# Kernel tuning notes

Hardware: AMD Instinct MI355X
Metric: run time of the kernel (lower is better)

Reference implementation:

```python
import jax, jax.numpy as jnp
import numpy as np

HEADS = 8
DIM_HEAD = 64
DIM = 512
HIDDEN = HEADS * DIM_HEAD  # 512


def setup_inputs() -> dict:
    key = jax.random.key(0)
    k1, k2, k3, k4 = jax.random.split(key, 4)
    B, H, W = 8, 64, 64
    x = jax.random.normal(k1, (B, DIM, H, W), dtype=jnp.float32)
    # Conv2d 1x1 weights stored as [out_ch, in_ch] (kernel 1x1 squeezed)
    w_qkv = jax.random.normal(k2, (3 * HIDDEN, DIM), dtype=jnp.float32) * (1.0 / np.sqrt(DIM))
    w_out = jax.random.normal(k3, (DIM, HIDDEN), dtype=jnp.float32) * (1.0 / np.sqrt(HIDDEN))
    b_out = jax.random.normal(k4, (DIM,), dtype=jnp.float32) * 0.01
    return {"x": x, "w_qkv": w_qkv, "w_out": w_out, "b_out": b_out}


def reference(x, w_qkv, w_out, b_out):
    b, c, h, w = x.shape
    n = h * w
    # to_qkv: 1x1 conv == channel GEMM
    qkv = jnp.einsum('bchw,oc->bohw', x, w_qkv)               # [b, 3*heads*dh, h, w]
    qkv = qkv.reshape(b, 3, HEADS, DIM_HEAD, n)               # split (qkv heads c), flatten (h w)
    q, k, v = qkv[:, 0], qkv[:, 1], qkv[:, 2]                 # each [b, heads, dh, n]
    k = jax.nn.softmax(k, axis=-1)                            # softmax over spatial tokens
    context = jnp.einsum('bhdn,bhen->bhde', k, v)             # [b, heads, dh, dh]
    out = jnp.einsum('bhde,bhdn->bhen', context, q)           # [b, heads, dh, n]
    out = out.reshape(b, HIDDEN, h, w)
    # to_out: 1x1 conv with bias
    return jnp.einsum('bchw,oc->bohw', out, w_out) + b_out[None, :, None, None]
```

## Files before the change

### kernel.cpp

```cpp
#include <hip/hip_runtime.h>
#include <hip/hip_bf16.h>


typedef __attribute__((ext_vector_type(8))) __bf16 bf16x8;
typedef __attribute__((ext_vector_type(4))) float f32x4;
typedef __attribute__((ext_vector_type(8))) unsigned short u16x8;
typedef __attribute__((ext_vector_type(4))) float float4v;

__device__ __forceinline__ unsigned short f2b(float f) {
  unsigned int u = __builtin_bit_cast(unsigned int, f);
  unsigned int r = (u + 0x7FFFu + ((u >> 16) & 1u)) >> 16;
  return (unsigned short)r;
}
__device__ __forceinline__ float b2f(unsigned short h) {
  unsigned int u = ((unsigned int)h) << 16;
  return __builtin_bit_cast(float, u);
}

__global__ __launch_bounds__(256) void prep_wkv_kernel(const float* __restrict__ w,
                                                       unsigned short* __restrict__ wkv) {
  int i = (blockIdx.x * 256 + threadIdx.x) * 4;
  const float* src = w + 512 * 512;
  #pragma unroll
  for (int j = 0; j < 4; ++j) wkv[i + j] = f2b(src[i + j]);
}

__global__ __launch_bounds__(256) void prep_wqT_kernel(const float* __restrict__ w,
                                                       unsigned short* __restrict__ WqT) {
  __shared__ unsigned short tile[64][65];
  const int ct = blockIdx.x, ot = blockIdx.y;
  const int c0 = ct * 64, o0 = ot * 64;
  const int tc = threadIdx.x & 63, tr = threadIdx.x >> 6;
  #pragma unroll
  for (int i = 0; i < 16; ++i) {
    int row = tr * 16 + i;
    tile[tc][row] = f2b(w[(long)(o0 + row) * 512 + c0 + tc]);
  }
  __syncthreads();
  #pragma unroll
  for (int i = 0; i < 16; ++i) {
    int row = tr * 16 + i;
    WqT[(long)(c0 + row) * 512 + o0 + tc] = tile[row][tc];
  }
}

__global__ __launch_bounds__(256) void transpose_x_kernel(const float* __restrict__ x,
                                                          unsigned short* __restrict__ xT) {
  __shared__ unsigned short tile[64][65];
  const int b = blockIdx.z, ct = blockIdx.y, nt = blockIdx.x;
  const int c0 = ct * 64, n0 = nt * 64;
  const int tid = threadIdx.x;

  const int n_off = (tid & 15) * 4;
  const float* xp = x + ((long)b * 512) * 4096 + n0;
  #pragma unroll
  for (int i = 0; i < 4; ++i) {
    int c_local = i * 16 + (tid >> 4);
    float4v v = *(const float4v*)(xp + (long)(c0 + c_local) * 4096 + n_off);
    #pragma unroll
    for (int j = 0; j < 4; ++j) tile[n_off + j][c_local] = f2b(v[j]);
  }
  __syncthreads();

  const int n_row = tid >> 2;
  const int c_seg = (tid & 3) * 16;
  unsigned short* xtp = xT + ((long)b * 4096 + n0 + n_row) * 512 + c0 + c_seg;
  #pragma unroll
  for (int s = 0; s < 2; ++s) {
    u16x8 o;
    #pragma unroll
    for (int k = 0; k < 8; ++k) o[k] = tile[n_row][c_seg + s * 8 + k];
    *(u16x8*)(xtp + s * 8) = o;
  }
}

__global__ __launch_bounds__(256) void gemm128_bt(
    const unsigned short* __restrict__ A, long strideA,
    const unsigned short* __restrict__ BT, long strideBT,
    void* __restrict__ Cout, long strideC, int ldc,
    const float* __restrict__ bias) {
  constexpr int K = 512;
  const int b = blockIdx.z;
  const int m0 = blockIdx.y * 128;
  const int n0 = blockIdx.x * 128;
  const unsigned short* Ab = A + (long)b * strideA;
  const unsigned short* Bb = BT + (long)b * strideBT;

  __shared__ unsigned short lds[2 * 128 * 64];
  char* ldsc = (char*)lds;

  const int tid = threadIdx.x;
  const int wave = tid >> 6;
  const int lane = tid & 63;
  const int wr = wave >> 1;
  const int wc = wave & 1;

  f32x4 acc[4][4];
  const f32x4 zero = {0.f, 0.f, 0.f, 0.f};
  #pragma unroll
  for (int i = 0; i < 4; ++i)
    #pragma unroll
    for (int j = 0; j < 4; ++j) acc[i][j] = zero;

  for (int kt = 0; kt < K; kt += 64) {
    #pragma unroll
    for (int q = 0; q < 4; ++q) {
      unsigned base = q * 4096 + wave * 1024;
      unsigned D = base + lane * 16;
      unsigned row = D >> 7;
      unsigned g = (D >> 4) & 7;
      unsigned gl = g ^ (row & 7);
      const unsigned short* srcA = Ab + (long)(m0 + row) * K + kt + gl * 8;
      __builtin_amdgcn_global_load_lds(
          (const __attribute__((address_space(1))) unsigned int*)srcA,
          (__attribute__((address_space(3))) unsigned int*)(ldsc + base), 16, 0, 0);
      const unsigned short* srcB = Bb + (long)(n0 + row) * K + kt + gl * 8;
      __builtin_amdgcn_global_load_lds(
          (const __attribute__((address_space(1))) unsigned int*)srcB,
          (__attribute__((address_space(3))) unsigned int*)(ldsc + 16384 + base), 16, 0, 0);
    }
    __syncthreads();

    bf16x8 af[2][4], bfr[2][4];
    #pragma unroll
    for (int ks = 0; ks < 2; ++ks) {
      #pragma unroll
      for (int mi = 0; mi < 4; ++mi) {
        unsigned row = wr * 64 + mi * 16 + (lane & 15);
        unsigned g = ((unsigned)(ks * 4 + (lane >> 4))) ^ (row & 7);
        af[ks][mi] = *(const bf16x8*)(ldsc + row * 128 + g * 16);
      }
      #pragma unroll
      for (int ni = 0; ni < 4; ++ni) {
        unsigned row = wc * 64 + ni * 16 + (lane & 15);
        unsigned g = ((unsigned)(ks * 4 + (lane >> 4))) ^ (row & 7);
        bfr[ks][ni] = *(const bf16x8*)(ldsc + 16384 + row * 128 + g * 16);
      }
    }
    #pragma unroll
    for (int ks = 0; ks < 2; ++ks)
      #pragma unroll
      for (int mi = 0; mi < 4; ++mi)
        #pragma unroll
        for (int ni = 0; ni < 4; ++ni)
          acc[mi][ni] = __builtin_amdgcn_mfma_f32_16x16x32_bf16(
              af[ks][mi], bfr[ks][ni], acc[mi][ni], 0, 0, 0);
    __syncthreads();
  }

  const int r0 = (lane >> 4) * 4;
  const int cn = lane & 15;
  if (bias != nullptr) {
    float* C = (float*)Cout + (long)b * strideC;
    #pragma unroll
    for (int mi = 0; mi < 4; ++mi) {
      int o = m0 + wr * 64 + mi * 16 + r0;
      #pragma unroll
      for (int ni = 0; ni < 4; ++ni) {
        int n = n0 + wc * 64 + ni * 16 + cn;
        #pragma unroll
        for (int r = 0; r < 4; ++r)
          C[(long)(o + r) * ldc + n] = acc[mi][ni][r] + bias[o + r];
      }
    }
  } else {
    unsigned short* C = (unsigned short*)Cout + (long)b * strideC;
    #pragma unroll
    for (int mi = 0; mi < 4; ++mi) {
      int o = m0 + wr * 64 + mi * 16 + r0;
      #pragma unroll
      for (int ni = 0; ni < 4; ++ni) {
        int n = n0 + wc * 64 + ni * 16 + cn;
        #pragma unroll
        for (int r = 0; r < 4; ++r)
          C[(long)(o + r) * ldc + n] = f2b(acc[mi][ni][r]);
      }
    }
  }
}

__global__ __launch_bounds__(256) void rowstat_kernel(const unsigned short* __restrict__ kv,
                                                      float* __restrict__ stats) {
  const int row = blockIdx.x;
  const int b = row >> 9, d = row & 511;
  const unsigned short* kp = kv + ((long)b * 1024 + d) * 4096;
  const int tid = threadIdx.x, wave = tid >> 6, lane = tid & 63;
  __shared__ float red[8];

  float v[16];
  u16x8 l0 = *(const u16x8*)(kp + tid * 8);
  u16x8 l1 = *(const u16x8*)(kp + 2048 + tid * 8);
  #pragma unroll
  for (int j = 0; j < 8; ++j) { v[j] = b2f(l0[j]); v[8 + j] = b2f(l1[j]); }

  float m = v[0];
  #pragma unroll
  for (int j = 1; j < 16; ++j) m = fmaxf(m, v[j]);
  #pragma unroll
  for (int off = 32; off > 0; off >>= 1) m = fmaxf(m, __shfl_xor(m, off));
  if (lane == 0) red[wave] = m;
  __syncthreads();
  m = fmaxf(fmaxf(red[0], red[1]), fmaxf(red[2], red[3]));

  float s = 0.f;
  #pragma unroll
  for (int j = 0; j < 16; ++j) s += __expf(v[j] - m);
  #pragma unroll
  for (int off = 32; off > 0; off >>= 1) s += __shfl_xor(s, off);
  if (lane == 0) red[4 + wave] = s;
  __syncthreads();
  if (tid == 0) {
    s = red[4] + red[5] + red[6] + red[7];
    stats[2 * row] = m;
    stats[2 * row + 1] = 1.0f / s;
  }
}

__global__ __launch_bounds__(256) void context_kernel(const unsigned short* __restrict__ kv,
                                                      const float* __restrict__ stats,
                                                      float* __restrict__ ctx_part) {
  const int s = blockIdx.x, bh = blockIdx.y, b = bh >> 3, h = bh & 7;
  const unsigned short* Kp = kv + ((long)b * 1024 + h * 64) * 4096;
  const unsigned short* Vp = kv + ((long)b * 1024 + 512 + h * 64) * 4096;
  const float* sb = stats + ((long)b * 512 + h * 64) * 2;
  const int tid = threadIdx.x, wave = tid >> 6, lane = tid & 63;

  float mrow[4], srow[4];
  #pragma unroll
  for (int mi = 0; mi < 4; ++mi) {
    int rA = mi * 16 + (lane & 15);
    mrow[mi] = sb[2 * rA];
    srow[mi] = sb[2 * rA + 1];
  }

  f32x4 acc[4][4];
  const f32x4 zero = {0.f, 0.f, 0.f, 0.f};
  #pragma unroll
  for (int i = 0; i < 4; ++i)
    #pragma unroll
    for (int j = 0; j < 4; ++j) acc[i][j] = zero;

  const int kbeg = s * 512 + wave * 128;
  for (int k0 = kbeg; k0 < kbeg + 128; k0 += 32) {
    const int kc = k0 + (lane >> 4) * 8;
    bf16x8 a[4], bv[4];
    #pragma unroll
    for (int mi = 0; mi < 4; ++mi) {
      u16x8 kr = *(const u16x8*)(Kp + (long)(mi * 16 + (lane & 15)) * 4096 + kc);
      u16x8 pr;
      #pragma unroll
      for (int j = 0; j < 8; ++j)
        pr[j] = f2b(__expf(b2f(kr[j]) - mrow[mi]) * srow[mi]);
      a[mi] = __builtin_bit_cast(bf16x8, pr);
    }
    #pragma unroll
    for (int ni = 0; ni < 4; ++ni)
      bv[ni] = *(const bf16x8*)(Vp + (long)(ni * 16 + (lane & 15)) * 4096 + kc);
    #pragma unroll
    for (int mi = 0; mi < 4; ++mi)
      #pragma unroll
      for (int ni = 0; ni < 4; ++ni)
        acc[mi][ni] = __builtin_amdgcn_mfma_f32_16x16x32_bf16(a[mi], bv[ni], acc[mi][ni], 0, 0, 0);
  }

  __shared__ float part[4][64][64];
  #pragma unroll
  for (int mi = 0; mi < 4; ++mi)
    #pragma unroll
    for (int ni = 0; ni < 4; ++ni)
      #pragma unroll
      for (int r = 0; r < 4; ++r)
        part[wave][mi * 16 + (lane >> 4) * 4 + r][ni * 16 + (lane & 15)] = acc[mi][ni][r];
  __syncthreads();
  float* cp = ctx_part + ((long)(s * 64 + bh)) * 4096;
  for (int i = tid; i < 4096; i += 256) {
    int dd = i >> 6, ee = i & 63;
    cp[i] = part[0][dd][ee] + part[1][dd][ee] + part[2][dd][ee] + part[3][dd][ee];
  }
}

__global__ __launch_bounds__(256) void w2_kernel(const float* __restrict__ ctx_part,
                                                 const float* __restrict__ w_out,
                                                 unsigned short* __restrict__ W2) {
  const int cq = blockIdx.x, bh = blockIdx.y, b = bh >> 3, h = bh & 7;
  __shared__ float cs[64][65];
  const int tid = threadIdx.x;
  for (int i = tid; i < 4096; i += 256) {
    float v = 0.f;
    #pragma unroll
    for (int s = 0; s < 8; ++s) v += ctx_part[((long)(s * 64 + bh)) * 4096 + i];
    cs[i >> 6][i & 63] = v;
  }
  __syncthreads();
  const int c = cq * 128 + (tid & 127);
  const int dbeg = (tid >> 7) * 32;
  const float* wp = w_out + (long)c * 512 + h * 64;
  float wrow[64];
  #pragma unroll
  for (int e = 0; e < 64; ++e) wrow[e] = wp[e];
  unsigned short* W2p = W2 + ((long)b * 512 + c) * 512 + h * 64;
  for (int dd = dbeg; dd < dbeg + 32; ++dd) {
    float s = 0.f;
    #pragma unroll
    for (int e = 0; e < 64; ++e) s = fmaf(wrow[e], cs[dd][e], s);
    W2p[dd] = f2b(s);
  }
}

extern "C" void kernel_launch(void* const* d_in, const int* in_sizes, int n_in,
                              void* d_out, int out_size, void* d_ws, size_t ws_size,
                              hipStream_t stream) {
  const float* x     = (const float*)d_in[0];
  const float* w_qkv = (const float*)d_in[1];
  const float* w_out = (const float*)d_in[2];
  const float* b_out = (const float*)d_in[3];

  char* ws = (char*)d_ws;
  unsigned short* xT   = (unsigned short*)ws;
  unsigned short* kv   = (unsigned short*)(ws + 33554432);
  unsigned short* wkv  = (unsigned short*)(ws + 100663296);
  unsigned short* WqT  = (unsigned short*)(ws + 101711872);
  float*          stats= (float*)(ws + 102236160);
  float*          ctxp = (float*)(ws + 102268928);
  unsigned short* W2   = (unsigned short*)(ws + 110657536);
  unsigned short* W3   = (unsigned short*)(ws + 114851840);

  prep_wkv_kernel<<<dim3(512), dim3(256), 0, stream>>>(w_qkv, wkv);
  prep_wqT_kernel<<<dim3(8, 8), dim3(256), 0, stream>>>(w_qkv, WqT);
  transpose_x_kernel<<<dim3(64, 8, 8), dim3(256), 0, stream>>>(x, xT);
  gemm128_bt<<<dim3(32, 8, 8), dim3(256), 0, stream>>>(
      wkv, 0L, xT, (long)4096 * 512, (void*)kv, (long)1024 * 4096, 4096, (const float*)nullptr);
  rowstat_kernel<<<dim3(4096), dim3(256), 0, stream>>>(kv, stats);
  context_kernel<<<dim3(8, 64), dim3(256), 0, stream>>>(kv, stats, ctxp);
  w2_kernel<<<dim3(4, 64), dim3(256), 0, stream>>>(ctxp, w_out, W2);
  gemm128_bt<<<dim3(4, 4, 8), dim3(256), 0, stream>>>(
      W2, (long)512 * 512, WqT, 0L, (void*)W3, (long)512 * 512, 512, (const float*)nullptr);
  gemm128_bt<<<dim3(32, 4, 8), dim3(256), 0, stream>>>(
      W3, (long)512 * 512, xT, (long)4096 * 512, d_out, (long)512 * 4096, 4096, b_out);
}
```

Baseline: 166.4 us.

## Fuse softmax row stats into single-block context kernel and use 64-row GEMM tiles

Removes the separate rowstat kernel by computing online max/sum for each K row inside a new per-(batch,head) context kernel that covers the full spatial range. This also drops the split-K partial buffer and its reduction in w2_kernel. The last two GEMMs switch to a new 64x128 tile kernel so more blocks are launched. The cost is that the context stage now runs only 64 blocks, each looping over 4096 tokens, which may underuse the GPU's compute units.

```diff
diff --git a/kernel.cpp b/kernel.cpp
--- a/kernel.cpp
+++ b/kernel.cpp
@@ -179,58 +179,161 @@
   }
 }
 
-__global__ __launch_bounds__(256) void rowstat_kernel(const unsigned short* __restrict__ kv,
-                                                      float* __restrict__ stats) {
-  const int row = blockIdx.x;
-  const int b = row >> 9, d = row & 511;
-  const unsigned short* kp = kv + ((long)b * 1024 + d) * 4096;
-  const int tid = threadIdx.x, wave = tid >> 6, lane = tid & 63;
-  __shared__ float red[8];
-
-  float v[16];
-  u16x8 l0 = *(const u16x8*)(kp + tid * 8);
-  u16x8 l1 = *(const u16x8*)(kp + 2048 + tid * 8);
-  #pragma unroll
-  for (int j = 0; j < 8; ++j) { v[j] = b2f(l0[j]); v[8 + j] = b2f(l1[j]); }
-
-  float m = v[0];
-  #pragma unroll
-  for (int j = 1; j < 16; ++j) m = fmaxf(m, v[j]);
-  #pragma unroll
-  for (int off = 32; off > 0; off >>= 1) m = fmaxf(m, __shfl_xor(m, off));
-  if (lane == 0) red[wave] = m;
-  __syncthreads();
-  m = fmaxf(fmaxf(red[0], red[1]), fmaxf(red[2], red[3]));
-
-  float s = 0.f;
-  #pragma unroll
-  for (int j = 0; j < 16; ++j) s += __expf(v[j] - m);
-  #pragma unroll
-  for (int off = 32; off > 0; off >>= 1) s += __shfl_xor(s, off);
-  if (lane == 0) red[4 + wave] = s;
-  __syncthreads();
-  if (tid == 0) {
-    s = red[4] + red[5] + red[6] + red[7];
-    stats[2 * row] = m;
-    stats[2 * row + 1] = 1.0f / s;
-  }
-}
-
-__global__ __launch_bounds__(256) void context_kernel(const unsigned short* __restrict__ kv,
-                                                      const float* __restrict__ stats,
-                                                      float* __restrict__ ctx_part) {
-  const int s = blockIdx.x, bh = blockIdx.y, b = bh >> 3, h = bh & 7;
+__global__ __launch_bounds__(256) void gemm64_bt(
+    const unsigned short* __restrict__ A, long strideA,
+    const unsigned short* __restrict__ BT, long strideBT,
+    void* __restrict__ Cout, long strideC, int ldc,
+    const float* __restrict__ bias) {
+  constexpr int K = 512;
+  const int b = blockIdx.z;
+  const int m0 = blockIdx.y * 64;
+  const int n0 = blockIdx.x * 128;
+  const unsigned short* Ab = A + (long)b * strideA;
+  const unsigned short* Bb = BT + (long)b * strideBT;
+
+  __shared__ unsigned short lds[(64 + 128) * 64];
+  char* ldsc = (char*)lds;
+
+  const int tid = threadIdx.x;
+  const int wave = tid >> 6;
+  const int lane = tid & 63;
+  const int wc = wave;
+
+  f32x4 acc[4][2];
+  const f32x4 zero = {0.f, 0.f, 0.f, 0.f};
+  #pragma unroll
+  for (int i = 0; i < 4; ++i)
+    #pragma unroll
+    for (int j = 0; j < 2; ++j) acc[i][j] = zero;
+
+  for (int kt = 0; kt < K; kt += 64) {
+    #pragma unroll
+    for (int q = 0; q < 2; ++q) {
+      unsigned base = q * 4096 + wave * 1024;
+      unsigned D = base + lane * 16;
+      unsigned row = D >> 7;
+      unsigned g = (D >> 4) & 7;
+      unsigned gl = g ^ (row & 7);
+      const unsigned short* srcA = Ab + (long)(m0 + row) * K + kt + gl * 8;
+      __builtin_amdgcn_global_load_lds(
+          (const __attribute__((address_space(1))) unsigned int*)srcA,
+          (__attribute__((address_space(3))) unsigned int*)(ldsc + base), 16, 0, 0);
+    }
+    #pragma unroll
+    for (int q = 0; q < 4; ++q) {
+      unsigned base = q * 4096 + wave * 1024;
+      unsigned D = base + lane * 16;
+      unsigned row = D >> 7;
+      unsigned g = (D >> 4) & 7;
+      unsigned gl = g ^ (row & 7);
+      const unsigned short* srcB = Bb + (long)(n0 + row) * K + kt + gl * 8;
+      __builtin_amdgcn_global_load_lds(
+          (const __attribute__((address_space(1))) unsigned int*)srcB,
+          (__attribute__((address_space(3))) unsigned int*)(ldsc + 8192 + base), 16, 0, 0);
+    }
+    __syncthreads();
+
+    bf16x8 af[2][4], bfr[2][2];
+    #pragma unroll
+    for (int ks = 0; ks < 2; ++ks) {
+      #pragma unroll
+      for (int mi = 0; mi < 4; ++mi) {
+        unsigned row = mi * 16 + (lane & 15);
+        unsigned g = ((unsigned)(ks * 4 + (lane >> 4))) ^ (row & 7);
+        af[ks][mi] = *(const bf16x8*)(ldsc + row * 128 + g * 16);
+      }
+      #pragma unroll
+      for (int ni = 0; ni < 2; ++ni) {
+        unsigned row = wc * 32 + ni * 16 + (lane & 15);
+        unsigned g = ((unsigned)(ks * 4 + (lane >> 4))) ^ (row & 7);
+        bfr[ks][ni] = *(const bf16x8*)(ldsc + 8192 + row * 128 + g * 16);
+      }
+    }
+    #pragma unroll
+    for (int ks = 0; ks < 2; ++ks)
+      #pragma unroll
+      for (int mi = 0; mi < 4; ++mi)
+        #pragma unroll
+        for (int ni = 0; ni < 2; ++ni)
+          acc[mi][ni] = __builtin_amdgcn_mfma_f32_16x16x32_bf16(
+              af[ks][mi], bfr[ks][ni], acc[mi][ni], 0, 0, 0);
+    __syncthreads();
+  }
+
+  const int r0 = (lane >> 4) * 4;
+  const int cn = lane & 15;
+  if (bias != nullptr) {
+    float* C = (float*)Cout + (long)b * strideC;
+    #pragma unroll
+    for (int mi = 0; mi < 4; ++mi) {
+      int o = m0 + mi * 16 + r0;
+      #pragma unroll
+      for (int ni = 0; ni < 2; ++ni) {
+        int n = n0 + wc * 32 + ni * 16 + cn;
+        #pragma unroll
+        for (int r = 0; r < 4; ++r)
+          C[(long)(o + r) * ldc + n] = acc[mi][ni][r] + bias[o + r];
+      }
+    }
+  } else {
+    unsigned short* C = (unsigned short*)Cout + (long)b * strideC;
+    #pragma unroll
+    for (int mi = 0; mi < 4; ++mi) {
+      int o = m0 + mi * 16 + r0;
+      #pragma unroll
+      for (int ni = 0; ni < 2; ++ni) {
+        int n = n0 + wc * 32 + ni * 16 + cn;
+        #pragma unroll
+        for (int r = 0; r < 4; ++r)
+          C[(long)(o + r) * ldc + n] = f2b(acc[mi][ni][r]);
+      }
+    }
+  }
+}
+
+__global__ __launch_bounds__(256) void context_full_kernel(const unsigned short* __restrict__ kv,
+                                                           float* __restrict__ ctx) {
+  const int bh = blockIdx.x, b = bh >> 3, h = bh & 7;
   const unsigned short* Kp = kv + ((long)b * 1024 + h * 64) * 4096;
   const unsigned short* Vp = kv + ((long)b * 1024 + 512 + h * 64) * 4096;
-  const float* sb = stats + ((long)b * 512 + h * 64) * 2;
   const int tid = threadIdx.x, wave = tid >> 6, lane = tid & 63;
+
+  __shared__ float sm[64], ss[64];
+
+  {
+    const int r = tid >> 2, sub = tid & 3;
+    const unsigned short* rp = Kp + (long)r * 4096 + sub * 8;
+    float m = -3.4e38f, s = 0.f;
+    #pragma unroll 4
+    for (int j = 0; j < 128; ++j) {
+      u16x8 v8 = *(const u16x8*)(rp + j * 32);
+      float v[8];
+      #pragma unroll
+      for (int i = 0; i < 8; ++i) v[i] = b2f(v8[i]);
+      float vm = fmaxf(fmaxf(fmaxf(v[0], v[1]), fmaxf(v[2], v[3])),
+                       fmaxf(fmaxf(v[4], v[5]), fmaxf(v[6], v[7])));
+      if (vm > m) { s *= __expf(m - vm); m = vm; }
+      #pragma unroll
+      for (int i = 0; i < 8; ++i) s += __expf(v[i] - m);
+    }
+    #pragma unroll
+    for (int off = 1; off <= 2; off <<= 1) {
+      float mo = __shfl_xor(m, off);
+      float so = __shfl_xor(s, off);
+      float mn = fmaxf(m, mo);
+      s = s * __expf(m - mn) + so * __expf(mo - mn);
+      m = mn;
+    }
+    if (sub == 0) { sm[r] = m; ss[r] = 1.0f / s; }
+  }
+  __syncthreads();
 
   float mrow[4], srow[4];
   #pragma unroll
   for (int mi = 0; mi < 4; ++mi) {
     int rA = mi * 16 + (lane & 15);
-    mrow[mi] = sb[2 * rA];
-    srow[mi] = sb[2 * rA + 1];
+    mrow[mi] = sm[rA];
+    srow[mi] = ss[rA];
   }
 
   f32x4 acc[4][4];
@@ -240,8 +343,8 @@
     #pragma unroll
     for (int j = 0; j < 4; ++j) acc[i][j] = zero;
 
-  const int kbeg = s * 512 + wave * 128;
-  for (int k0 = kbeg; k0 < kbeg + 128; k0 += 32) {
+  const int kbeg = wave * 1024;
+  for (int k0 = kbeg; k0 < kbeg + 1024; k0 += 32) {
     const int kc = k0 + (lane >> 4) * 8;
     bf16x8 a[4], bv[4];
     #pragma unroll
@@ -272,25 +375,20 @@
       for (int r = 0; r < 4; ++r)
         part[wave][mi * 16 + (lane >> 4) * 4 + r][ni * 16 + (lane & 15)] = acc[mi][ni][r];
   __syncthreads();
-  float* cp = ctx_part + ((long)(s * 64 + bh)) * 4096;
+  float* cp = ctx + (long)bh * 4096;
   for (int i = tid; i < 4096; i += 256) {
     int dd = i >> 6, ee = i & 63;
     cp[i] = part[0][dd][ee] + part[1][dd][ee] + part[2][dd][ee] + part[3][dd][ee];
   }
 }
 
-__global__ __launch_bounds__(256) void w2_kernel(const float* __restrict__ ctx_part,
+__global__ __launch_bounds__(256) void w2_kernel(const float* __restrict__ ctx,
                                                  const float* __restrict__ w_out,
                                                  unsigned short* __restrict__ W2) {
   const int cq = blockIdx.x, bh = blockIdx.y, b = bh >> 3, h = bh & 7;
   __shared__ float cs[64][65];
   const int tid = threadIdx.x;
-  for (int i = tid; i < 4096; i += 256) {
-    float v = 0.f;
-    #pragma unroll
-    for (int s = 0; s < 8; ++s) v += ctx_part[((long)(s * 64 + bh)) * 4096 + i];
-    cs[i >> 6][i & 63] = v;
-  }
+  for (int i = tid; i < 4096; i += 256) cs[i >> 6][i & 63] = ctx[(long)bh * 4096 + i];
   __syncthreads();
   const int c = cq * 128 + (tid & 127);
   const int dbeg = (tid >> 7) * 32;
@@ -320,8 +418,7 @@
   unsigned short* kv   = (unsigned short*)(ws + 33554432);
   unsigned short* wkv  = (unsigned short*)(ws + 100663296);
   unsigned short* WqT  = (unsigned short*)(ws + 101711872);
-  float*          stats= (float*)(ws + 102236160);
-  float*          ctxp = (float*)(ws + 102268928);
+  float*          ctx  = (float*)(ws + 102268928);
   unsigned short* W2   = (unsigned short*)(ws + 110657536);
   unsigned short* W3   = (unsigned short*)(ws + 114851840);
 
@@ -330,11 +427,10 @@
   transpose_x_kernel<<<dim3(64, 8, 8), dim3(256), 0, stream>>>(x, xT);
   gemm128_bt<<<dim3(32, 8, 8), dim3(256), 0, stream>>>(
       wkv, 0L, xT, (long)4096 * 512, (void*)kv, (long)1024 * 4096, 4096, (const float*)nullptr);
-  rowstat_kernel<<<dim3(4096), dim3(256), 0, stream>>>(kv, stats);
-  context_kernel<<<dim3(8, 64), dim3(256), 0, stream>>>(kv, stats, ctxp);
-  w2_kernel<<<dim3(4, 64), dim3(256), 0, stream>>>(ctxp, w_out, W2);
-  gemm128_bt<<<dim3(4, 4, 8), dim3(256), 0, stream>>>(
+  context_full_kernel<<<dim3(64), dim3(256), 0, stream>>>(kv, ctx);
+  w2_kernel<<<dim3(4, 64), dim3(256), 0, stream>>>(ctx, w_out, W2);
+  gemm64_bt<<<dim3(4, 8, 8), dim3(256), 0, stream>>>(
       W2, (long)512 * 512, WqT, 0L, (void*)W3, (long)512 * 512, 512, (const float*)nullptr);
-  gemm128_bt<<<dim3(32, 4, 8), dim3(256), 0, stream>>>(
+  gemm64_bt<<<dim3(32, 8, 8), dim3(256), 0, stream>>>(
       W3, (long)512 * 512, xT, (long)4096 * 512, d_out, (long)512 * 4096, 4096, b_out);
 }
```

New measurement: 193.1 us. 16.1% more time.
